# Kernel optimization log

Measured on AMD Instinct MI355X. Metric: run time of the kernel, lower is better.

Reference implementation:

```python
import jax, jax.numpy as jnp
import numpy as np

IN_DIM, OUT_DIM = 1024, 1024
GRID_SIZE, K = 8, 3
TOKENS = 8192


def b_splines(x, grid, k):
    # x: [B, in_dim], grid: [in_dim, grid_size + 2k + 1]
    x = x[..., None]  # [B, in_dim, 1]
    # order-0 indicator bases: [B, in_dim, grid_size + 2k]
    bases = ((x >= grid[:, :-1]) & (x < grid[:, 1:])).astype(x.dtype)
    # Cox-de Boor recursion up to order k -> [B, in_dim, grid_size + k]
    for kk in range(1, k + 1):
        left = (x - grid[:, : -(kk + 1)]) / (grid[:, kk:-1] - grid[:, : -(kk + 1)])
        right = (grid[:, kk + 1:] - x) / (grid[:, kk + 1:] - grid[:, 1:-kk])
        bases = left * bases[..., :-1] + right * bases[..., 1:]
    return bases


def setup_inputs() -> dict:
    key = jax.random.key(0)
    k1, k2, k3 = jax.random.split(key, 3)
    x = jax.random.normal(k1, (TOKENS, IN_DIM), dtype=jnp.float32)
    # grid buffer: arange(-k, grid_size+k+1) * step + grid_range[0], repeated per in_dim
    grid_range = (-1.0, 1.0)
    step = (grid_range[1] - grid_range[0]) / GRID_SIZE
    grid_row = np.arange(-K, GRID_SIZE + K + 1, dtype=np.float32) * step + grid_range[0]
    grid = jnp.asarray(np.tile(grid_row, (IN_DIM, 1)))  # [in_dim, 15]
    coeff = jax.random.normal(k2, (OUT_DIM, IN_DIM, GRID_SIZE + K), dtype=jnp.float32) * 0.1
    scale_base = 1.0 / np.sqrt(IN_DIM) + jax.random.normal(k3, (OUT_DIM, IN_DIM), dtype=jnp.float32) * 0.1
    scale_spline = jnp.ones((1,), dtype=jnp.float32)
    return {"x": x, "grid": grid, "coeff": coeff, "scale_base": scale_base,
            "scale_spline": scale_spline}


def reference(x, grid, coeff, scale_base, scale_spline):
    splines = b_splines(x, grid, K)                      # [B, in, G+K]
    y_b = jnp.matmul(jax.nn.silu(x), scale_base.T)       # [B, out]
    w = coeff * scale_spline                             # scalar broadcast [out, in, G+K]
    y_spline = jnp.einsum('big,oig->bo', splines, w)     # [B, out]
    return y_b + y_spline
```

## Files before the change

kernel.cpp:

```cpp
#include <hip/hip_runtime.h>
#include <hip/hip_bf16.h>
#include <stdint.h>

typedef __attribute__((ext_vector_type(8))) short short8;
typedef __attribute__((ext_vector_type(16))) float floatx16;
typedef unsigned short u16;

#define IN_DIM  1024
#define OUT_DIM 1024
#define NG      11
#define GK      12
#define KDIM    (IN_DIM * GK)
#define TOKENS  8192
#define MT      64
#define BK      96
#define PB      104
#define NOPS    26

__device__ __forceinline__ u16 f2bf(float f) {
  uint32_t u = __float_as_uint(f);
  uint32_t r = (u + 0x7fffu + ((u >> 16) & 1u)) >> 16;
  return (u16)r;
}

__global__ __launch_bounds__(256) void pack_wt_kernel(
    const float* __restrict__ coeff, const float* __restrict__ sb,
    const float* __restrict__ ss_p, u16* __restrict__ Wt)
{
  __shared__ float cf[256 * NG];
  __shared__ __align__(16) u16 st[256 * GK];
  const int tid = threadIdx.x;
  const int b   = blockIdx.x;
  const int o   = b >> 2;
  const int i0  = (b & 3) * 256;
  const float* cbase = coeff + (size_t)o * (IN_DIM * NG) + (size_t)i0 * NG;
#pragma unroll
  for (int p = 0; p < NG; ++p) cf[p * 256 + tid] = cbase[p * 256 + tid];
  const float ss  = ss_p[0];
  const float sbv = sb[(size_t)o * IN_DIM + i0 + tid];
  __syncthreads();
  const float* cp = cf + tid * NG;
  u16 h[GK];
#pragma unroll
  for (int g = 0; g < NG; ++g) h[g] = f2bf(cp[g] * ss);
  h[NG] = f2bf(sbv);
  uint64_t V0 = (uint64_t)h[0] | ((uint64_t)h[1] << 16) | ((uint64_t)h[2] << 32) | ((uint64_t)h[3] << 48);
  uint64_t V1 = (uint64_t)h[4] | ((uint64_t)h[5] << 16) | ((uint64_t)h[6] << 32) | ((uint64_t)h[7] << 48);
  uint64_t V2 = (uint64_t)h[8] | ((uint64_t)h[9] << 16) | ((uint64_t)h[10] << 32) | ((uint64_t)h[11] << 48);
  uint64_t* sp = (uint64_t*)(st + tid * GK);
  sp[0] = V0; sp[1] = V1; sp[2] = V2;
  __syncthreads();
  const uint4* src = (const uint4*)st;
  uint4* dst = (uint4*)(Wt + (size_t)b * (256 * GK));
  dst[tid] = src[tid];
  if (tid < 128) dst[256 + tid] = src[256 + tid];
}

__device__ __forceinline__ void expand_regs(float x, float g0, float inv_h,
                                            uint64_t& V0, uint64_t& V1, uint64_t& V2)
{
  float t  = (x - g0) * inv_h;
  float fc = floorf(t);
  int   c  = (int)fc;
  float u  = t - fc;
  float u2 = u * u;
  float w1 = 1.0f - u;
  float b0 = (w1 * w1 * w1) * (1.0f / 6.0f);
  float b1 = (0.5f * u - 1.0f) * u2 + (2.0f / 3.0f);
  float b2 = ((-0.5f * u + 0.5f) * u + 0.5f) * u + (1.0f / 6.0f);
  float b3 = (u2 * u) * (1.0f / 6.0f);
  float sil = x / (1.0f + __expf(-x));

  uint64_t P = (uint64_t)f2bf(b0) | ((uint64_t)f2bf(b1) << 16)
             | ((uint64_t)f2bf(b2) << 32) | ((uint64_t)f2bf(b3) << 48);
  int  k  = c - 3;
  bool cv = (c >= 0) && (c <= 13);
  int  kneg = (k < 0) ? -k : 0;
  uint64_t Pc = cv ? (P >> (16 * kneg)) : 0ull;
  uint32_t sh = (uint32_t)(16 * ((k < 0) ? 0 : k));

  V0 = (sh < 64)  ? (Pc << (sh & 63)) : 0ull;
  V1 = (sh == 0)  ? 0ull :
       (sh < 64)  ? (Pc >> ((64 - sh) & 63)) :
       (sh < 128) ? (Pc << ((sh - 64) & 63)) : 0ull;
  V2 = (sh <= 64) ? 0ull :
       (sh < 128) ? (Pc >> ((128 - sh) & 63)) :
                    (Pc << ((sh - 128) & 63));
  V2 = (V2 & 0x0000FFFFFFFFFFFFull) | ((uint64_t)f2bf(sil) << 48);
}

__device__ __forceinline__ void async16(const u16* g, u16* l) {
  __builtin_amdgcn_global_load_lds(
      (const __attribute__((address_space(1))) uint32_t*)g,
      (__attribute__((address_space(3))) uint32_t*)l,
      16, 0, 0);
}

__global__ __launch_bounds__(256, 3) void gemm_fused_kernel(
    const float* __restrict__ X, const float* __restrict__ grid,
    const u16* __restrict__ Wt, float* __restrict__ out, float* __restrict__ part,
    int k_iters)
{
  __shared__ __align__(16) u16 As[128 * PB];
  __shared__ __align__(16) u16 Bs[128 * PB];

  const int tid  = threadIdx.x;
  const int lane = tid & 63;
  const int wave = tid >> 6;
  const int mt8  = MT * 8;
  const int s    = blockIdx.x / mt8;
  const int r    = blockIdx.x - s * mt8;
  const int bm   = r % MT;
  const int bn   = r / MT;
  const int wm = (wave >> 1) * 64;
  const int wn = (wave & 1) * 64;

  const float g0    = grid[0];
  const float inv_h = 1.0f / (grid[1] - grid[0]);

  floatx16 acc[2][2];
#pragma unroll
  for (int a = 0; a < 2; ++a)
#pragma unroll
    for (int b = 0; b < 2; ++b)
#pragma unroll
      for (int rr = 0; rr < 16; ++rr) acc[a][b][rr] = 0.f;

  const int kb_u16 = s * k_iters * BK;
  const u16* bsrc[7];
  u16*       bdst[7];
  bool       bact[7];
#pragma unroll
  for (int j = 0; j < 7; ++j) {
    int o  = wave + 4 * j;
    bact[j] = (o < NOPS);
    int oc = bact[j] ? o : (NOPS - 1);
    int gidx  = oc * 64 + lane;
    int row   = gidx / 13;
    int chunk = gidx - row * 13;
    int c8    = (chunk == 12) ? 0 : chunk;
    bsrc[j] = Wt + (size_t)(bn * 128 + row) * KDIM + kb_u16 + c8 * 8;
    bdst[j] = Bs + oc * 512;
  }

  const int arow = tid & 127;
  const int half = tid >> 7;
  const float* xp = X + (size_t)(bm * 128 + arow) * IN_DIM + s * (k_iters * 8) + half * 4;
  uint4* awp = (uint4*)(As + arow * PB + half * 48);

  const int l31 = lane & 31;
  const int g   = lane >> 5;

  float4 xv = *(const float4*)xp;

  for (int it = 0; it < k_iters; ++it) {
    uint64_t ev[12];
    expand_regs(xv.x, g0, inv_h, ev[0], ev[1], ev[2]);
    expand_regs(xv.y, g0, inv_h, ev[3], ev[4], ev[5]);
    expand_regs(xv.z, g0, inv_h, ev[6], ev[7], ev[8]);
    expand_regs(xv.w, g0, inv_h, ev[9], ev[10], ev[11]);
    if (it + 1 < k_iters) xv = *(const float4*)(xp + (size_t)(it + 1) * 8);

    __syncthreads();

#pragma unroll
    for (int j = 0; j < 7; ++j)
      if (bact[j]) async16(bsrc[j] + (size_t)it * BK, bdst[j]);

#pragma unroll
    for (int j = 0; j < 6; ++j) {
      uint4 w;
      w.x = (uint32_t)ev[2*j];     w.y = (uint32_t)(ev[2*j] >> 32);
      w.z = (uint32_t)ev[2*j+1];   w.w = (uint32_t)(ev[2*j+1] >> 32);
      awp[j] = w;
    }

    __syncthreads();

#pragma unroll
    for (int t = 0; t < 6; ++t) {
      const int cc = 2 * t + g;
      short8 af[2], bf[2];
#pragma unroll
      for (int ss2 = 0; ss2 < 2; ++ss2) {
        af[ss2] = *(const short8*)&As[(wm + ss2 * 32 + l31) * PB + cc * 8];
        bf[ss2] = *(const short8*)&Bs[(wn + ss2 * 32 + l31) * PB + cc * 8];
      }
#pragma unroll
      for (int sm = 0; sm < 2; ++sm)
#pragma unroll
        for (int sn = 0; sn < 2; ++sn)
          acc[sm][sn] = __builtin_amdgcn_mfma_f32_32x32x16_bf16(af[sm], bf[sn], acc[sm][sn], 0, 0, 0);
    }
  }
  __syncthreads();

  float* op = (s == 0) ? out : part;
#pragma unroll
  for (int sm = 0; sm < 2; ++sm)
#pragma unroll
    for (int sn = 0; sn < 2; ++sn) {
      const int row0 = bm * 128 + wm + sm * 32 + 4 * g;
      const int col  = bn * 128 + wn + sn * 32 + l31;
#pragma unroll
      for (int reg = 0; reg < 16; ++reg) {
        int row = row0 + (reg & 3) + 8 * (reg >> 2);
        op[(size_t)row * OUT_DIM + col] = acc[sm][sn][reg];
      }
    }
}

__global__ __launch_bounds__(256) void reduce_kernel(
    float* __restrict__ out, const float* __restrict__ part)
{
  size_t i = (size_t)blockIdx.x * 256 + threadIdx.x;
  float4* o = (float4*)out;
  const float4* p = (const float4*)part;
  float4 a = o[i], b = p[i];
  a.x += b.x; a.y += b.y; a.z += b.z; a.w += b.w;
  o[i] = a;
}

extern "C" void kernel_launch(void* const* d_in, const int* in_sizes, int n_in,
                              void* d_out, int out_size, void* d_ws, size_t ws_size,
                              hipStream_t stream) {
  const float* x     = (const float*)d_in[0];
  const float* grid  = (const float*)d_in[1];
  const float* coeff = (const float*)d_in[2];
  const float* sb    = (const float*)d_in[3];
  const float* ss    = (const float*)d_in[4];
  float* out = (float*)d_out;

  u16* Wt = (u16*)d_ws;
  const size_t wt_bytes   = (size_t)OUT_DIM * KDIM * 2;
  const size_t part_bytes = (size_t)TOKENS * OUT_DIM * 4;
  float* part = (float*)((char*)d_ws + wt_bytes);

  pack_wt_kernel<<<(OUT_DIM * IN_DIM) / 256, 256, 0, stream>>>(coeff, sb, ss, Wt);

  if (ws_size >= wt_bytes + part_bytes) {
    gemm_fused_kernel<<<MT * 8 * 2, 256, 0, stream>>>(x, grid, Wt, out, part, 64);
    reduce_kernel<<<(TOKENS * OUT_DIM / 4) / 256, 256, 0, stream>>>(out, part);
  } else {
    gemm_fused_kernel<<<MT * 8, 256, 0, stream>>>(x, grid, Wt, out, nullptr, 128);
  }
}
```

Baseline: 417.1 us.

## Pre-expand spline bases into bf16 matrix and run plain split-K GEMM

```diff
diff --git a/kernel.cpp b/kernel.cpp
--- a/kernel.cpp
+++ b/kernel.cpp
@@ -16,6 +16,7 @@
 #define BK      96
 #define PB      104
 #define NOPS    26
+#define GBK     64
 
 __device__ __forceinline__ u16 f2bf(float f) {
   uint32_t u = __float_as_uint(f);
@@ -96,6 +97,127 @@
       16, 0, 0);
 }
 
+__global__ __launch_bounds__(256) void expand_x_kernel(
+    const float* __restrict__ X, const float* __restrict__ grid,
+    u16* __restrict__ Aexp)
+{
+  __shared__ __align__(16) uint4 st[1536];
+  const int tid = threadIdx.x;
+  const int row = blockIdx.x;
+  const float g0    = grid[0];
+  const float inv_h = 1.0f / (grid[1] - grid[0]);
+
+  float4 xv = *(const float4*)(X + (size_t)row * IN_DIM + tid * 4);
+  uint64_t ev[12];
+  expand_regs(xv.x, g0, inv_h, ev[0], ev[1], ev[2]);
+  expand_regs(xv.y, g0, inv_h, ev[3], ev[4], ev[5]);
+  expand_regs(xv.z, g0, inv_h, ev[6], ev[7], ev[8]);
+  expand_regs(xv.w, g0, inv_h, ev[9], ev[10], ev[11]);
+#pragma unroll
+  for (int j = 0; j < 6; ++j) {
+    uint4 w;
+    w.x = (uint32_t)ev[2*j];     w.y = (uint32_t)(ev[2*j] >> 32);
+    w.z = (uint32_t)ev[2*j+1];   w.w = (uint32_t)(ev[2*j+1] >> 32);
+    st[tid * 6 + j] = w;
+  }
+  __syncthreads();
+  uint4* dst = (uint4*)(Aexp + (size_t)row * KDIM);
+#pragma unroll
+  for (int j = 0; j < 6; ++j) dst[j * 256 + tid] = st[j * 256 + tid];
+}
+
+__global__ __launch_bounds__(256, 3) void gemm_pre_kernel(
+    const u16* __restrict__ A, const u16* __restrict__ Wt,
+    float* __restrict__ out, float* __restrict__ part, int k_iters)
+{
+  __shared__ __align__(16) u16 As[128 * GBK];
+  __shared__ __align__(16) u16 Bs[128 * GBK];
+
+  const int tid  = threadIdx.x;
+  const int lane = tid & 63;
+  const int wave = tid >> 6;
+  const int s    = blockIdx.x >> 9;
+  const int r    = blockIdx.x & 511;
+  const int bm   = r >> 3;
+  const int bn   = r & 7;
+  const int wm   = (wave >> 1) * 64;
+  const int wn   = (wave & 1) * 64;
+  const int l31  = lane & 31;
+  const int g8   = lane >> 5;
+
+  floatx16 acc[2][2];
+#pragma unroll
+  for (int a = 0; a < 2; ++a)
+#pragma unroll
+    for (int b = 0; b < 2; ++b)
+#pragma unroll
+      for (int rr = 0; rr < 16; ++rr) acc[a][b][rr] = 0.f;
+
+  const size_t k0 = (size_t)s * k_iters * GBK;
+  const u16* asrc[4]; const u16* bsrc[4]; u16* adst[4]; u16* bdst[4];
+#pragma unroll
+  for (int o = 0; o < 4; ++o) {
+    int idx = o * 256 + tid;
+    int rw = idx >> 3, c = idx & 7;
+    asrc[o] = A  + (size_t)(bm * 128 + rw) * KDIM + k0 + c * 8;
+    bsrc[o] = Wt + (size_t)(bn * 128 + rw) * KDIM + k0 + c * 8;
+    adst[o] = As + idx * 8;
+    bdst[o] = Bs + idx * 8;
+  }
+
+  for (int it = 0; it < k_iters; ++it) {
+    __syncthreads();
+#pragma unroll
+    for (int o = 0; o < 4; ++o) async16(asrc[o], adst[o]);
+#pragma unroll
+    for (int o = 0; o < 4; ++o) async16(bsrc[o], bdst[o]);
+#pragma unroll
+    for (int o = 0; o < 4; ++o) { asrc[o] += GBK; bsrc[o] += GBK; }
+    __syncthreads();
+
+#pragma unroll
+    for (int t = 0; t < 4; ++t) {
+      short8 af[2], bf[2];
+#pragma unroll
+      for (int ss2 = 0; ss2 < 2; ++ss2) {
+        af[ss2] = *(const short8*)&As[(wm + ss2 * 32 + l31) * GBK + t * 16 + g8 * 8];
+        bf[ss2] = *(const short8*)&Bs[(wn + ss2 * 32 + l31) * GBK + t * 16 + g8 * 8];
+      }
+#pragma unroll
+      for (int sm = 0; sm < 2; ++sm)
+#pragma unroll
+        for (int sn = 0; sn < 2; ++sn)
+          acc[sm][sn] = __builtin_amdgcn_mfma_f32_32x32x16_bf16(af[sm], bf[sn], acc[sm][sn], 0, 0, 0);
+    }
+  }
+
+  float* op = (s == 0) ? out : (part + (size_t)(s - 1) * TOKENS * OUT_DIM);
+#pragma unroll
+  for (int sm = 0; sm < 2; ++sm)
+#pragma unroll
+    for (int sn = 0; sn < 2; ++sn) {
+      const int row0 = bm * 128 + wm + sm * 32 + 4 * g8;
+      const int col  = bn * 128 + wn + sn * 32 + l31;
+#pragma unroll
+      for (int reg = 0; reg < 16; ++reg) {
+        int row = row0 + (reg & 3) + 8 * (reg >> 2);
+        op[(size_t)row * OUT_DIM + col] = acc[sm][sn][reg];
+      }
+    }
+}
+
+__global__ __launch_bounds__(256) void reduce3_kernel(
+    float* __restrict__ out, const float* __restrict__ part)
+{
+  size_t i = (size_t)blockIdx.x * 256 + threadIdx.x;
+  float4* o = (float4*)out;
+  const float4* p = (const float4*)part;
+  const size_t n4 = (size_t)TOKENS * OUT_DIM / 4;
+  float4 a = o[i], b = p[i], c = p[i + n4];
+  a.x += b.x + c.x; a.y += b.y + c.y; a.z += b.z + c.z; a.w += b.w + c.w;
+  o[i] = a;
+}
+
 __global__ __launch_bounds__(256, 3) void gemm_fused_kernel(
     const float* __restrict__ X, const float* __restrict__ grid,
     const u16* __restrict__ Wt, float* __restrict__ out, float* __restrict__ part,
@@ -233,12 +355,23 @@
 
   u16* Wt = (u16*)d_ws;
   const size_t wt_bytes   = (size_t)OUT_DIM * KDIM * 2;
+  const size_t aexp_bytes = (size_t)TOKENS * KDIM * 2;
   const size_t part_bytes = (size_t)TOKENS * OUT_DIM * 4;
-  float* part = (float*)((char*)d_ws + wt_bytes);
 
   pack_wt_kernel<<<(OUT_DIM * IN_DIM) / 256, 256, 0, stream>>>(coeff, sb, ss, Wt);
 
-  if (ws_size >= wt_bytes + part_bytes) {
+  if (ws_size >= wt_bytes + aexp_bytes + 2 * part_bytes) {
+    u16*   Aexp = (u16*)((char*)d_ws + wt_bytes);
+    float* part = (float*)((char*)d_ws + wt_bytes + aexp_bytes);
+    expand_x_kernel<<<TOKENS, 256, 0, stream>>>(x, grid, Aexp);
+    gemm_pre_kernel<<<512 * 3, 256, 0, stream>>>(Aexp, Wt, out, part, 64);
+    reduce3_kernel<<<(TOKENS * OUT_DIM / 4) / 256, 256, 0, stream>>>(out, part);
+  } else if (ws_size >= wt_bytes + aexp_bytes) {
+    u16* Aexp = (u16*)((char*)d_ws + wt_bytes);
+    expand_x_kernel<<<TOKENS, 256, 0, stream>>>(x, grid, Aexp);
+    gemm_pre_kernel<<<512, 256, 0, stream>>>(Aexp, Wt, out, nullptr, 192);
+  } else if (ws_size >= wt_bytes + part_bytes) {
+    float* part = (float*)((char*)d_ws + wt_bytes);
     gemm_fused_kernel<<<MT * 8 * 2, 256, 0, stream>>>(x, grid, Wt, out, part, 64);
     reduce_kernel<<<(TOKENS * OUT_DIM / 4) / 256, 256, 0, stream>>>(out, part);
   } else {
```

After: 581.0 us. 1.39x slower.

## Rewrite fused KAN GEMM with 256x256 tiles, 8 waves and double-buffered async pipeline

Applied to the files above, without the earlier changes.

```diff
diff --git a/kernel.cpp b/kernel.cpp
--- a/kernel.cpp
+++ b/kernel.cpp
@@ -12,10 +12,10 @@
 #define GK      12
 #define KDIM    (IN_DIM * GK)
 #define TOKENS  8192
-#define MT      64
-#define BK      96
-#define PB      104
-#define NOPS    26
+#define FBK     48
+#define FROW    56
+#define FBUF    (256 * FROW)
+#define FOPS    4
 
 __device__ __forceinline__ u16 f2bf(float f) {
   uint32_t u = __float_as_uint(f);
@@ -96,116 +96,152 @@
       16, 0, 0);
 }
 
-__global__ __launch_bounds__(256, 3) void gemm_fused_kernel(
+__device__ __forceinline__ void expand2(float2 xv, float g0, float inv_h, uint64_t e[6]) {
+  expand_regs(xv.x, g0, inv_h, e[0], e[1], e[2]);
+  expand_regs(xv.y, g0, inv_h, e[3], e[4], e[5]);
+}
+
+__device__ __forceinline__ void write_ev(u16* abase, int awoff, const uint64_t e[6]) {
+  uint4* w = (uint4*)(abase + awoff);
+  uint4 w0, w1, w2;
+  w0.x = (uint32_t)e[0]; w0.y = (uint32_t)(e[0] >> 32);
+  w0.z = (uint32_t)e[1]; w0.w = (uint32_t)(e[1] >> 32);
+  w1.x = (uint32_t)e[2]; w1.y = (uint32_t)(e[2] >> 32);
+  w1.z = (uint32_t)e[3]; w1.w = (uint32_t)(e[3] >> 32);
+  w2.x = (uint32_t)e[4]; w2.y = (uint32_t)(e[4] >> 32);
+  w2.z = (uint32_t)e[5]; w2.w = (uint32_t)(e[5] >> 32);
+  w[0] = w0; w[1] = w1; w[2] = w2;
+}
+
+__global__ __launch_bounds__(512, 2) void gemm_fused2_kernel(
     const float* __restrict__ X, const float* __restrict__ grid,
     const u16* __restrict__ Wt, float* __restrict__ out, float* __restrict__ part,
     int k_iters)
 {
-  __shared__ __align__(16) u16 As[128 * PB];
-  __shared__ __align__(16) u16 Bs[128 * PB];
+  __shared__ __align__(16) u16 S[4 * FBUF];
 
   const int tid  = threadIdx.x;
   const int lane = tid & 63;
   const int wave = tid >> 6;
-  const int mt8  = MT * 8;
-  const int s    = blockIdx.x / mt8;
-  const int r    = blockIdx.x - s * mt8;
-  const int bm   = r % MT;
-  const int bn   = r / MT;
-  const int wm = (wave >> 1) * 64;
-  const int wn = (wave & 1) * 64;
+  const int s    = blockIdx.x >> 7;
+  const int r    = blockIdx.x & 127;
+  const int bm   = r & 31;
+  const int bn   = r >> 5;
+  const int wm   = (wave >> 2) * 128;
+  const int wn   = (wave & 3) * 64;
+  const int l31  = lane & 31;
+  const int g8   = lane >> 5;
 
   const float g0    = grid[0];
   const float inv_h = 1.0f / (grid[1] - grid[0]);
 
-  floatx16 acc[2][2];
-#pragma unroll
-  for (int a = 0; a < 2; ++a)
+  floatx16 acc[4][2];
+#pragma unroll
+  for (int a = 0; a < 4; ++a)
 #pragma unroll
     for (int b = 0; b < 2; ++b)
 #pragma unroll
       for (int rr = 0; rr < 16; ++rr) acc[a][b][rr] = 0.f;
 
-  const int kb_u16 = s * k_iters * BK;
-  const u16* bsrc[7];
-  u16*       bdst[7];
-  bool       bact[7];
-#pragma unroll
-  for (int j = 0; j < 7; ++j) {
-    int o  = wave + 4 * j;
-    bact[j] = (o < NOPS);
-    int oc = bact[j] ? o : (NOPS - 1);
-    int gidx  = oc * 64 + lane;
-    int row   = gidx / 13;
-    int chunk = gidx - row * 13;
-    int c8    = (chunk == 12) ? 0 : chunk;
-    bsrc[j] = Wt + (size_t)(bn * 128 + row) * KDIM + kb_u16 + c8 * 8;
-    bdst[j] = Bs + oc * 512;
-  }
-
-  const int arow = tid & 127;
-  const int half = tid >> 7;
-  const float* xp = X + (size_t)(bm * 128 + arow) * IN_DIM + s * (k_iters * 8) + half * 4;
-  uint4* awp = (uint4*)(As + arow * PB + half * 48);
-
-  const int l31 = lane & 31;
-  const int g   = lane >> 5;
-
-  float4 xv = *(const float4*)xp;
-
-  for (int it = 0; it < k_iters; ++it) {
-    uint64_t ev[12];
-    expand_regs(xv.x, g0, inv_h, ev[0], ev[1], ev[2]);
-    expand_regs(xv.y, g0, inv_h, ev[3], ev[4], ev[5]);
-    expand_regs(xv.z, g0, inv_h, ev[6], ev[7], ev[8]);
-    expand_regs(xv.w, g0, inv_h, ev[9], ev[10], ev[11]);
-    if (it + 1 < k_iters) xv = *(const float4*)(xp + (size_t)(it + 1) * 8);
-
-    __syncthreads();
-
-#pragma unroll
-    for (int j = 0; j < 7; ++j)
-      if (bact[j]) async16(bsrc[j] + (size_t)it * BK, bdst[j]);
-
-#pragma unroll
-    for (int j = 0; j < 6; ++j) {
-      uint4 w;
-      w.x = (uint32_t)ev[2*j];     w.y = (uint32_t)(ev[2*j] >> 32);
-      w.z = (uint32_t)ev[2*j+1];   w.w = (uint32_t)(ev[2*j+1] >> 32);
-      awp[j] = w;
+  const int kb = s * k_iters * FBK;
+  const u16* bsrc[FOPS]; int bdof[FOPS];
+#pragma unroll
+  for (int j = 0; j < FOPS; ++j) {
+    int o  = wave + 8 * j;
+    int oc = (o < 28) ? o : 27;
+    int gidx = oc * 64 + lane;
+    int row  = gidx / 7;
+    int sl   = gidx - row * 7;
+    int c6   = (sl == 6) ? 0 : sl;
+    bsrc[j] = Wt + (size_t)(bn * 256 + row) * KDIM + kb + c6 * 8;
+    bdof[j] = oc * 512;
+  }
+
+  const int arow  = tid >> 1;
+  const int cp    = (tid & 1) * 2;
+  const float* xp = X + (size_t)(bm * 256 + arow) * IN_DIM + s * (k_iters * 4) + cp;
+  const int awoff = arow * FROW + cp * 12;
+
+  const int NT = k_iters;
+
+  float2 x0    = *(const float2*)(xp + 0);
+  float2 x1    = *(const float2*)(xp + 4);
+  float2 x_use = *(const float2*)(xp + 8);
+  float2 x_mid = *(const float2*)(xp + 12);
+  float2 x_new = x_use;
+
+#pragma unroll
+  for (int j = 0; j < FOPS; ++j) async16(bsrc[j],       S + 2 * FBUF + bdof[j]);
+#pragma unroll
+  for (int j = 0; j < FOPS; ++j) async16(bsrc[j] + FBK, S + 3 * FBUF + bdof[j]);
+  {
+    uint64_t e[6];
+    expand2(x0, g0, inv_h, e); write_ev(S, awoff, e);
+    expand2(x1, g0, inv_h, e); write_ev(S + FBUF, awoff, e);
+  }
+  asm volatile("s_waitcnt vmcnt(0) lgkmcnt(0)" ::: "memory");
+  __builtin_amdgcn_s_barrier();
+  __builtin_amdgcn_sched_barrier(0);
+
+  for (int t = 0; t < NT; ++t) {
+    const int p = t & 1;
+    const u16* Ab = S + p * FBUF;
+    const u16* Bb = S + 2 * FBUF + p * FBUF;
+
+    uint64_t e[6];
+    const bool dostage = (t + 2 < NT);
+    if (dostage) expand2(x_use, g0, inv_h, e);
+
+    __builtin_amdgcn_s_setprio(1);
+#pragma unroll
+    for (int ks = 0; ks < 3; ++ks) {
+      const int cc = (2 * ks + g8) * 8;
+      short8 bf0 = *(const short8*)&Bb[(wn +      l31) * FROW + cc];
+      short8 bf1 = *(const short8*)&Bb[(wn + 32 + l31) * FROW + cc];
+#pragma unroll
+      for (int m = 0; m < 4; ++m) {
+        short8 af = *(const short8*)&Ab[(wm + m * 32 + l31) * FROW + cc];
+        acc[m][0] = __builtin_amdgcn_mfma_f32_32x32x16_bf16(af, bf0, acc[m][0], 0, 0, 0);
+        acc[m][1] = __builtin_amdgcn_mfma_f32_32x32x16_bf16(af, bf1, acc[m][1], 0, 0, 0);
+      }
     }
-
-    __syncthreads();
-
-#pragma unroll
-    for (int t = 0; t < 6; ++t) {
-      const int cc = 2 * t + g;
-      short8 af[2], bf[2];
-#pragma unroll
-      for (int ss2 = 0; ss2 < 2; ++ss2) {
-        af[ss2] = *(const short8*)&As[(wm + ss2 * 32 + l31) * PB + cc * 8];
-        bf[ss2] = *(const short8*)&Bs[(wn + ss2 * 32 + l31) * PB + cc * 8];
+    __builtin_amdgcn_s_setprio(0);
+
+    __builtin_amdgcn_s_barrier();
+    __builtin_amdgcn_sched_barrier(0);
+
+    if (dostage) {
+      const int ko = (t + 2) * FBK;
+      u16* Bd = S + 2 * FBUF + p * FBUF;
+#pragma unroll
+      for (int j = 0; j < FOPS; ++j) async16(bsrc[j] + ko, Bd + bdof[j]);
+      write_ev(S + p * FBUF, awoff, e);
+      if (t + 4 < NT) {
+        x_new = *(const float2*)(xp + (size_t)(t + 4) * 4);
+        asm volatile("s_waitcnt vmcnt(5) lgkmcnt(0)" ::: "memory");
+      } else {
+        asm volatile("s_waitcnt vmcnt(4) lgkmcnt(0)" ::: "memory");
       }
-#pragma unroll
-      for (int sm = 0; sm < 2; ++sm)
-#pragma unroll
-        for (int sn = 0; sn < 2; ++sn)
-          acc[sm][sn] = __builtin_amdgcn_mfma_f32_32x32x16_bf16(af[sm], bf[sn], acc[sm][sn], 0, 0, 0);
+    } else {
+      asm volatile("s_waitcnt vmcnt(0) lgkmcnt(0)" ::: "memory");
     }
-  }
-  __syncthreads();
+    __builtin_amdgcn_s_barrier();
+    __builtin_amdgcn_sched_barrier(0);
+
+    x_use = x_mid; x_mid = x_new;
+  }
 
   float* op = (s == 0) ? out : part;
 #pragma unroll
-  for (int sm = 0; sm < 2; ++sm)
-#pragma unroll
-    for (int sn = 0; sn < 2; ++sn) {
-      const int row0 = bm * 128 + wm + sm * 32 + 4 * g;
-      const int col  = bn * 128 + wn + sn * 32 + l31;
+  for (int m = 0; m < 4; ++m)
+#pragma unroll
+    for (int n = 0; n < 2; ++n) {
+      const int row0 = bm * 256 + wm + m * 32 + 4 * g8;
+      const int col  = bn * 256 + wn + n * 32 + l31;
 #pragma unroll
       for (int reg = 0; reg < 16; ++reg) {
         int row = row0 + (reg & 3) + 8 * (reg >> 2);
-        op[(size_t)row * OUT_DIM + col] = acc[sm][sn][reg];
+        op[(size_t)row * OUT_DIM + col] = acc[m][n][reg];
       }
     }
 }
@@ -234,14 +270,14 @@
   u16* Wt = (u16*)d_ws;
   const size_t wt_bytes   = (size_t)OUT_DIM * KDIM * 2;
   const size_t part_bytes = (size_t)TOKENS * OUT_DIM * 4;
-  float* part = (float*)((char*)d_ws + wt_bytes);
 
   pack_wt_kernel<<<(OUT_DIM * IN_DIM) / 256, 256, 0, stream>>>(coeff, sb, ss, Wt);
 
   if (ws_size >= wt_bytes + part_bytes) {
-    gemm_fused_kernel<<<MT * 8 * 2, 256, 0, stream>>>(x, grid, Wt, out, part, 64);
+    float* part = (float*)((char*)d_ws + wt_bytes);
+    gemm_fused2_kernel<<<128 * 2, 512, 0, stream>>>(x, grid, Wt, out, part, 128);
     reduce_kernel<<<(TOKENS * OUT_DIM / 4) / 256, 256, 0, stream>>>(out, part);
   } else {
-    gemm_fused_kernel<<<MT * 8, 256, 0, stream>>>(x, grid, Wt, out, nullptr, 128);
-  }
-}
+    gemm_fused2_kernel<<<128, 512, 0, stream>>>(x, grid, Wt, out, nullptr, 256);
+  }
+}
```

After: 430.1 us. +3.1%, slower.
